# Kernel optimization log

Measured on AMD Instinct MI355X. Metric: run time of the kernel, lower is better.

The kernel has to match this reference:

```python
import jax, jax.numpy as jnp
import numpy as np

B, C, H, W = 8, 64, 64, 64
T, G, HID = 8, 8, 64


def setup_inputs() -> dict:
    key = jax.random.key(0)
    ks = jax.random.split(key, 8)
    s = 0.05
    return {
        "h": jax.random.normal(ks[0], (B, C, H, W), jnp.float32),
        "w_in": jax.random.normal(ks[1], (G * T, C), jnp.float32) * s,
        "b_in": jnp.zeros((G * T,), jnp.float32),
        "w_ih": jax.random.normal(ks[2], (4 * HID, 1), jnp.float32) * s,
        "w_hh": jax.random.normal(ks[3], (4 * HID, HID), jnp.float32) * s,
        "b_ih": jnp.zeros((4 * HID,), jnp.float32),
        "b_hh": jnp.zeros((4 * HID,), jnp.float32),
        "w_s": jax.random.normal(ks[4], (1, HID), jnp.float32) * s,
        "b_s": jnp.zeros((1,), jnp.float32),
        "w_out": jax.random.normal(ks[5], (C, G * T), jnp.float32) * s,
        "b_out": jnp.zeros((C,), jnp.float32),
    }


def reference(h, w_in, b_in, w_ih, w_hh, b_ih, b_hh, w_s, b_s, w_out, b_out):
    Bb, Cc, Hh, Ww = h.shape
    # 1x1 conv in-projection: (B,C,H,W) -> (B,G*T,H,W)
    y = jnp.einsum('bchw,oc->bohw', h, w_in) + b_in[None, :, None, None]
    y = y.reshape(Bb, G, T, Hh, Ww)
    # (B,G,H,W,T) -> (N,T) scalar sequences
    seq = jnp.transpose(y, (0, 1, 3, 4, 2)).reshape(-1, T)
    N = seq.shape[0]
    xs = seq.T  # (T, N) time-major for scan
    bias = b_ih + b_hh  # (4H,)
    w_x = w_ih[:, 0]    # (4H,) scalar-input weights

    def step(carry, x_t):
        hprev, cprev = carry
        # gates: i, f, g, o in torch LSTM ordering
        gates = x_t[:, None] * w_x[None, :] + hprev @ w_hh.T + bias  # (N,4H)
        i, f, g, o = jnp.split(gates, 4, axis=1)
        i = jax.nn.sigmoid(i)
        f = jax.nn.sigmoid(f)
        o = jax.nn.sigmoid(o)
        g = jnp.tanh(g)
        c = f * cprev + i * g
        hn = o * jnp.tanh(c)
        s_t = hn @ w_s[0] + b_s[0]  # fused to_scalar: (N,)
        return (hn, c), s_t

    init = (jnp.zeros((N, HID), h.dtype), jnp.zeros((N, HID), h.dtype))
    _, s = jax.lax.scan(step, init, xs)  # s: (T, N)

    out = s.T.reshape(Bb, G, Hh, Ww, T)
    out = jnp.transpose(out, (0, 1, 4, 2, 3)).reshape(Bb, G * T, Hh, Ww)
    # 1x1 conv out-projection back to C channels
    out = jnp.einsum('bchw,oc->bohw', out, w_out) + b_out[None, :, None, None]
    return out
```

## Files before the change

kernel.cpp:

```cpp
#include <hip/hip_runtime.h>
#include <hip/hip_bf16.h>

#define HW    4096
#define BB    8
#define TT    8

constexpr int OFF_WFRAG = 0;
constexpr int OFF_WXB   = 12800;

constexpr float SI = -1.44269504088896340736f;
constexpr float SG =  2.88539008177792681472f;

typedef _Float16 halfx8 __attribute__((ext_vector_type(8)));
typedef _Float16 halfx4 __attribute__((ext_vector_type(4)));
typedef float    floatx4 __attribute__((ext_vector_type(4)));
typedef float    floatx2 __attribute__((ext_vector_type(2)));

__device__ inline float fast_exp2(float x) {
#if __has_builtin(__builtin_amdgcn_exp2f)
    return __builtin_amdgcn_exp2f(x);
#else
    return __builtin_exp2f(x);
#endif
}
__device__ inline float fast_rcp(float x) {
#if __has_builtin(__builtin_amdgcn_rcpf)
    return __builtin_amdgcn_rcpf(x);
#else
    return 1.0f / x;
#endif
}
__device__ inline floatx2 exp2x2(floatx2 x) {
    floatx2 r; r.x = fast_exp2(x.x); r.y = fast_exp2(x.y); return r;
}
__device__ inline floatx2 rcpx2(floatx2 x) {
    float R = fast_rcp(x.x * x.y);
    floatx2 r; r.x = R * x.y; r.y = R * x.x; return r;
}

union pack8 { _Float16 h[8]; uint4 u; };

__global__ __launch_bounds__(256) void prep_kernel(
    const float* __restrict__ w_ih,  const float* __restrict__ w_hh,
    const float* __restrict__ b_ih,  const float* __restrict__ b_hh,
    const float* __restrict__ w_s,   const float* __restrict__ w_out,
    float* __restrict__ ws_f) {
    int tid = threadIdx.x;
    int bid = blockIdx.x;
    if (bid < 9) {
        int e = bid * 256 + tid;
        uint4* wf = (uint4*)(ws_f + OFF_WFRAG);
        if (e < 2048) {
            int l  = e & 63;
            int fi = e >> 6;
            int nb = fi >> 1, kc = fi & 1;
            int hb = nb & 3, gi = nb >> 2;
            int gate = gi * 64 + 4 * (l & 15) + hb;
            int hid  = kc * 32 + (l >> 4) * 8;
            float sc = (gi == 2) ? SG : SI;
            const float* src = w_hh + gate * 64 + hid;
            pack8 p;
            #pragma unroll
            for (int j = 0; j < 8; ++j) p.h[j] = (_Float16)(src[j] * sc);
            wf[e] = p.u;
        } else if (e < 2176) {
            int t2 = e - 2048;
            int l = t2 & 63, kc = t2 >> 6;
            pack8 p;
            #pragma unroll
            for (int j = 0; j < 8; ++j) p.h[j] = (_Float16)0.0f;
            if ((l & 15) == 0) {
                #pragma unroll
                for (int j = 0; j < 8; ++j)
                    p.h[j] = (_Float16)w_s[kc * 32 + (l >> 4) * 8 + j];
            }
            wf[e] = p.u;
        }
    } else {
        int s_ = tid & 15, hb = (tid >> 4) & 3, gi = tid >> 6;
        int gate = gi * 64 + 4 * s_ + hb;
        float sc = (gi == 2) ? SG : SI;
        floatx2 v; v.x = w_ih[gate] * sc; v.y = (b_ih[gate] + b_hh[gate]) * sc;
        ((floatx2*)(ws_f + OFF_WXB))[tid] = v;
    }
}

__global__ __launch_bounds__(512) void lstm_kernel(
    const float* __restrict__ hin,
    const float* __restrict__ ws_f,
    float* __restrict__ out,
    const float* __restrict__ w_in,
    const float* __restrict__ b_in,
    const float* __restrict__ b_s_p,
    const float* __restrict__ b_out,
    const float* __restrict__ w_out) {
    __shared__ uint4 wfrag_lds[2176];
    __shared__ floatx2 wxb_lds[256];
    __shared__ __align__(16) float x_lds[1024];
    __shared__ __align__(16) _Float16 h_lds[9216];
    __shared__ __align__(16) float stile[1024];
    __shared__ __align__(16) float wt_lds[4096];

    int tid = threadIdx.x;
    int ptile = blockIdx.x & 255;
    int b     = blockIdx.x >> 8;
    int p0 = ptile * 16;

    int lane = tid & 63;
    int wv   = tid >> 6;
    int g    = wv;
    int s    = lane & 15;
    int q    = lane >> 4;

    const uint4* wfg = (const uint4*)(ws_f + OFF_WFRAG);
    #pragma unroll
    for (int i = 0; i < 5; ++i) {
        int e = tid + 512 * i;
        if (e < 2176) wfrag_lds[e] = wfg[e];
    }
    if (tid < 256) wxb_lds[tid] = ((const floatx2*)(ws_f + OFF_WXB))[tid];
    #pragma unroll
    for (int i = 0; i < 2; ++i)
        ((floatx4*)wt_lds)[tid + 512 * i] = ((const floatx4*)w_in)[tid + 512 * i];
    if (tid < 256) {
        int cc = tid >> 2, f4 = tid & 3;
        ((floatx4*)stile)[tid] = *(const floatx4*)&hin[(b * 64 + cc) * HW + p0 + f4 * 4];
    }
    __syncthreads();

    {
        floatx2 xacc; xacc.x = b_in[g * 8 + q]; xacc.y = b_in[g * 8 + q + 4];
        #pragma unroll 8
        for (int cc = 0; cc < 64; ++cc) {
            float hv = stile[cc * 16 + s];
            floatx2 w;
            w.x = wt_lds[(g * 8 + q) * 64 + cc];
            w.y = wt_lds[(g * 8 + q + 4) * 64 + cc];
            floatx2 h2; h2.x = hv; h2.y = hv;
            xacc = xacc + w * h2;
        }
        x_lds[g * 128 + q * 16 + s]       = xacc.x;
        x_lds[g * 128 + (q + 4) * 16 + s] = xacc.y;
    }
    #pragma unroll
    for (int i = 0; i < 9; ++i)
        ((unsigned*)h_lds)[tid + 512 * i] = 0u;
    __syncthreads();

    #pragma unroll
    for (int i = 0; i < 2; ++i)
        ((floatx4*)wt_lds)[tid + 512 * i] = ((const floatx4*)w_out)[tid + 512 * i];

    _Float16* hrow = h_lds + wv * 16 * 72;
    float bs = b_s_p[0];

    float c_st[4][4];
    #pragma unroll
    for (int hb = 0; hb < 4; ++hb)
        #pragma unroll
        for (int r = 0; r < 4; ++r) c_st[hb][r] = 0.0f;

    for (int t = 0; t < TT; ++t) {
        asm volatile("" ::: "memory");

        halfx8 a0 = *(const halfx8*)(hrow + s * 72 + q * 8);
        halfx8 a1 = *(const halfx8*)(hrow + s * 72 + q * 8 + 32);

        if (t > 0) {
            halfx8 sb0 = *(const halfx8*)&wfrag_lds[32 * 64 + lane];
            halfx8 sb1 = *(const halfx8*)&wfrag_lds[33 * 64 + lane];
            floatx4 sa = {0.f, 0.f, 0.f, 0.f};
            sa = __builtin_amdgcn_mfma_f32_16x16x32_f16(a0, sb0, sa, 0, 0, 0);
            sa = __builtin_amdgcn_mfma_f32_16x16x32_f16(a1, sb1, sa, 0, 0, 0);
            if (s == 0) {
                floatx4 o4 = {sa[0] + bs, sa[1] + bs, sa[2] + bs, sa[3] + bs};
                *(floatx4*)&stile[(g * 8 + (t - 1)) * 16 + q * 4] = o4;
            }
        }

        floatx4 xv = *(const floatx4*)&x_lds[g * 128 + t * 16 + q * 4];
        floatx2 xlo; xlo.x = xv[0]; xlo.y = xv[1];
        floatx2 xhi; xhi.x = xv[2]; xhi.y = xv[3];

        halfx4 hpack[4];

        #pragma unroll
        for (int hb = 0; hb < 4; ++hb) {
            floatx4 acc[4];
            #pragma unroll
            for (int gi = 0; gi < 4; ++gi) {
                int nb = hb + 4 * gi;
                floatx2 wb = wxb_lds[s + 16 * nb];
                floatx2 lo = xlo * wb.x + wb.y;
                floatx2 hi = xhi * wb.x + wb.y;
                floatx4 a = {lo.x, lo.y, hi.x, hi.y};
                halfx8 b0 = *(const halfx8*)&wfrag_lds[(nb * 2 + 0) * 64 + lane];
                halfx8 b1 = *(const halfx8*)&wfrag_lds[(nb * 2 + 1) * 64 + lane];
                a = __builtin_amdgcn_mfma_f32_16x16x32_f16(a0, b0, a, 0, 0, 0);
                a = __builtin_amdgcn_mfma_f32_16x16x32_f16(a1, b1, a, 0, 0, 0);
                acc[gi] = a;
            }
            #pragma unroll
            for (int p = 0; p < 2; ++p) {
                int r0 = 2 * p;
                floatx2 Ei; Ei.x = fast_exp2(acc[0][r0]); Ei.y = fast_exp2(acc[0][r0 + 1]);
                floatx2 Ef; Ef.x = fast_exp2(acc[1][r0]); Ef.y = fast_exp2(acc[1][r0 + 1]);
                floatx2 Eg; Eg.x = fast_exp2(acc[2][r0]); Eg.y = fast_exp2(acc[2][r0 + 1]);
                floatx2 Eo; Eo.x = fast_exp2(acc[3][r0]); Eo.y = fast_exp2(acc[3][r0 + 1]);
                floatx2 Bf  = Ef + 1.0f;
                floatx2 Pig = (Ei + 1.0f) * (Eg + 1.0f);
                floatx2 cp; cp.x = c_st[hb][r0]; cp.y = c_st[hb][r0 + 1];
                floatx2 num = cp * Pig + (Eg * SG - SG) * Bf;
                floatx2 cs  = num * rcpx2(Bf * Pig);
                c_st[hb][r0] = cs.x; c_st[hb][r0 + 1] = cs.y;
                floatx2 Ec  = exp2x2(cs);
                floatx2 hn  = (Ec - 1.0f) * rcpx2((Eo + 1.0f) * (Ec + 1.0f));
                hpack[r0 + 0][hb] = (_Float16)hn.x;
                hpack[r0 + 1][hb] = (_Float16)hn.y;
            }
        }
        {
            _Float16* wp = hrow + (q * 4) * 72 + 4 * s;
            *(halfx4*)(wp +   0) = hpack[0];
            *(halfx4*)(wp +  72) = hpack[1];
            *(halfx4*)(wp + 144) = hpack[2];
            *(halfx4*)(wp + 216) = hpack[3];
        }
    }
    {
        asm volatile("" ::: "memory");
        halfx8 a0 = *(const halfx8*)(hrow + s * 72 + q * 8);
        halfx8 a1 = *(const halfx8*)(hrow + s * 72 + q * 8 + 32);
        halfx8 sb0 = *(const halfx8*)&wfrag_lds[32 * 64 + lane];
        halfx8 sb1 = *(const halfx8*)&wfrag_lds[33 * 64 + lane];
        floatx4 sa = {0.f, 0.f, 0.f, 0.f};
        sa = __builtin_amdgcn_mfma_f32_16x16x32_f16(a0, sb0, sa, 0, 0, 0);
        sa = __builtin_amdgcn_mfma_f32_16x16x32_f16(a1, sb1, sa, 0, 0, 0);
        if (s == 0) {
            floatx4 o4 = {sa[0] + bs, sa[1] + bs, sa[2] + bs, sa[3] + bs};
            *(floatx4*)&stile[(g * 8 + 7) * 16 + q * 4] = o4;
        }
    }
    __syncthreads();

    {
        int px = tid & 15;
        int oo = tid >> 4;
        floatx2 acc; acc.x = b_out[oo]; acc.y = b_out[oo + 32];
        #pragma unroll
        for (int c4 = 0; c4 < 16; ++c4) {
            floatx4 w0 = *(const floatx4*)&wt_lds[oo * 64 + c4 * 4];
            floatx4 w1 = *(const floatx4*)&wt_lds[(oo + 32) * 64 + c4 * 4];
            #pragma unroll
            for (int j = 0; j < 4; ++j) {
                float sv = stile[(c4 * 4 + j) * 16 + px];
                acc.x += w0[j] * sv;
                acc.y += w1[j] * sv;
            }
        }
        out[(b * 64 + oo) * HW + p0 + px]      = acc.x;
        out[(b * 64 + oo + 32) * HW + p0 + px] = acc.y;
    }
}

extern "C" void kernel_launch(void* const* d_in, const int* in_sizes, int n_in,
                              void* d_out, int out_size, void* d_ws, size_t ws_size,
                              hipStream_t stream) {
    const float* h     = (const float*)d_in[0];
    const float* w_in  = (const float*)d_in[1];
    const float* b_in  = (const float*)d_in[2];
    const float* w_ih  = (const float*)d_in[3];
    const float* w_hh  = (const float*)d_in[4];
    const float* b_ih  = (const float*)d_in[5];
    const float* b_hh  = (const float*)d_in[6];
    const float* w_s   = (const float*)d_in[7];
    const float* b_s   = (const float*)d_in[8];
    const float* w_out = (const float*)d_in[9];
    const float* b_out = (const float*)d_in[10];
    float* out = (float*)d_out;
    float* ws  = (float*)d_ws;

    prep_kernel<<<10, 256, 0, stream>>>(w_ih, w_hh, b_ih, b_hh, w_s, w_out, ws);
    lstm_kernel<<<2048, 512, 0, stream>>>(h, ws, out, w_in, b_in, b_s, b_out, w_out);
}
```

Baseline: 226.3 us.

## Process two pixel tiles per 1024-thread block with XOR-swizzled h buffer

Each block now handles two 16-pixel tiles using 1024 threads, so the LSTM weight fragments staged in LDS are shared across twice the work and the block count halves. The padded h layout is replaced by an XOR-swizzled 64-wide layout to avoid bank conflicts while using less padding. The w_in and w_out matrices are no longer staged in LDS and are read from global/cache directly, and the input and scalar-output tiles share a single buffer. The trade-off is larger blocks with more register and LDS pressure per block, plus uncached global weight reads in the projection loops.

```diff
diff --git a/kernel.cpp b/kernel.cpp
--- a/kernel.cpp
+++ b/kernel.cpp
@@ -85,7 +85,7 @@
     }
 }
 
-__global__ __launch_bounds__(512) void lstm_kernel(
+__global__ __launch_bounds__(1024) void lstm_kernel(
     const float* __restrict__ hin,
     const float* __restrict__ ws_f,
     float* __restrict__ out,
@@ -96,63 +96,62 @@
     const float* __restrict__ w_out) {
     __shared__ uint4 wfrag_lds[2176];
     __shared__ floatx2 wxb_lds[256];
-    __shared__ __align__(16) float x_lds[1024];
-    __shared__ __align__(16) _Float16 h_lds[9216];
-    __shared__ __align__(16) float stile[1024];
-    __shared__ __align__(16) float wt_lds[4096];
+    __shared__ __align__(16) float xs_buf[2048];
+    __shared__ __align__(16) _Float16 h_lds[16384];
 
     int tid = threadIdx.x;
-    int ptile = blockIdx.x & 255;
-    int b     = blockIdx.x >> 8;
-    int p0 = ptile * 16;
-
     int lane = tid & 63;
     int wv   = tid >> 6;
-    int g    = wv;
+    int tl   = wv >> 3;
+    int g    = wv & 7;
     int s    = lane & 15;
     int q    = lane >> 4;
 
+    int gt = blockIdx.x * 2 + tl;
+    int b  = gt >> 8;
+    int p0 = (gt & 255) * 16;
+
     const uint4* wfg = (const uint4*)(ws_f + OFF_WFRAG);
     #pragma unroll
-    for (int i = 0; i < 5; ++i) {
-        int e = tid + 512 * i;
+    for (int i = 0; i < 3; ++i) {
+        int e = tid + 1024 * i;
         if (e < 2176) wfrag_lds[e] = wfg[e];
     }
     if (tid < 256) wxb_lds[tid] = ((const floatx2*)(ws_f + OFF_WXB))[tid];
-    #pragma unroll
-    for (int i = 0; i < 2; ++i)
-        ((floatx4*)wt_lds)[tid + 512 * i] = ((const floatx4*)w_in)[tid + 512 * i];
-    if (tid < 256) {
-        int cc = tid >> 2, f4 = tid & 3;
-        ((floatx4*)stile)[tid] = *(const floatx4*)&hin[(b * 64 + cc) * HW + p0 + f4 * 4];
-    }
-    __syncthreads();
-
+    if (tid < 512) {
+        int tls = tid >> 8, cc = (tid >> 2) & 63, f4 = tid & 3;
+        int gts = blockIdx.x * 2 + tls;
+        int bs_ = gts >> 8, p0s = (gts & 255) * 16;
+        ((floatx4*)h_lds)[tid] =
+            *(const floatx4*)&hin[(bs_ * 64 + cc) * HW + p0s + f4 * 4];
+    }
+    __syncthreads();
+
+    float* xs = xs_buf + tl * 1024 + g * 128;
     {
+        const float* hin_st = (const float*)h_lds + tl * 1024;
+        const float* wrow0 = w_in + (g * 8 + q) * 64;
+        const float* wrow1 = w_in + (g * 8 + q + 4) * 64;
         floatx2 xacc; xacc.x = b_in[g * 8 + q]; xacc.y = b_in[g * 8 + q + 4];
         #pragma unroll 8
         for (int cc = 0; cc < 64; ++cc) {
-            float hv = stile[cc * 16 + s];
-            floatx2 w;
-            w.x = wt_lds[(g * 8 + q) * 64 + cc];
-            w.y = wt_lds[(g * 8 + q + 4) * 64 + cc];
-            floatx2 h2; h2.x = hv; h2.y = hv;
-            xacc = xacc + w * h2;
-        }
-        x_lds[g * 128 + q * 16 + s]       = xacc.x;
-        x_lds[g * 128 + (q + 4) * 16 + s] = xacc.y;
-    }
+            float hv = hin_st[cc * 16 + s];
+            xacc.x += wrow0[cc] * hv;
+            xacc.y += wrow1[cc] * hv;
+        }
+        xs[q * 16 + s]       = xacc.x;
+        xs[(q + 4) * 16 + s] = xacc.y;
+    }
+    __syncthreads();
     #pragma unroll
-    for (int i = 0; i < 9; ++i)
-        ((unsigned*)h_lds)[tid + 512 * i] = 0u;
-    __syncthreads();
-
-    #pragma unroll
-    for (int i = 0; i < 2; ++i)
-        ((floatx4*)wt_lds)[tid + 512 * i] = ((const floatx4*)w_out)[tid + 512 * i];
-
-    _Float16* hrow = h_lds + wv * 16 * 72;
+    for (int i = 0; i < 8; ++i)
+        ((unsigned*)h_lds)[tid + 1024 * i] = 0u;
+    __syncthreads();
+
+    _Float16* hrow = h_lds + wv * 1024;
     float bs = b_s_p[0];
+    int sh8 = (s >> 1);
+    int so4 = 4 * (s & 1);
 
     float c_st[4][4];
     #pragma unroll
@@ -163,8 +162,8 @@
     for (int t = 0; t < TT; ++t) {
         asm volatile("" ::: "memory");
 
-        halfx8 a0 = *(const halfx8*)(hrow + s * 72 + q * 8);
-        halfx8 a1 = *(const halfx8*)(hrow + s * 72 + q * 8 + 32);
+        halfx8 a0 = *(const halfx8*)(hrow + s * 64 + 8 * (q ^ (s & 7)));
+        halfx8 a1 = *(const halfx8*)(hrow + s * 64 + 8 * ((q + 4) ^ (s & 7)));
 
         if (t > 0) {
             halfx8 sb0 = *(const halfx8*)&wfrag_lds[32 * 64 + lane];
@@ -174,11 +173,11 @@
             sa = __builtin_amdgcn_mfma_f32_16x16x32_f16(a1, sb1, sa, 0, 0, 0);
             if (s == 0) {
                 floatx4 o4 = {sa[0] + bs, sa[1] + bs, sa[2] + bs, sa[3] + bs};
-                *(floatx4*)&stile[(g * 8 + (t - 1)) * 16 + q * 4] = o4;
-            }
-        }
-
-        floatx4 xv = *(const floatx4*)&x_lds[g * 128 + t * 16 + q * 4];
+                *(floatx4*)&xs[(t - 1) * 16 + q * 4] = o4;
+            }
+        }
+
+        floatx4 xv = *(const floatx4*)&xs[t * 16 + q * 4];
         floatx2 xlo; xlo.x = xv[0]; xlo.y = xv[1];
         floatx2 xhi; xhi.x = xv[2]; xhi.y = xv[3];
 
@@ -220,17 +219,18 @@
             }
         }
         {
-            _Float16* wp = hrow + (q * 4) * 72 + 4 * s;
-            *(halfx4*)(wp +   0) = hpack[0];
-            *(halfx4*)(wp +  72) = hpack[1];
-            *(halfx4*)(wp + 144) = hpack[2];
-            *(halfx4*)(wp + 216) = hpack[3];
+            int rowb = q * 4;
+            #pragma unroll
+            for (int r = 0; r < 4; ++r) {
+                int row = rowb + r;
+                *(halfx4*)(hrow + row * 64 + 8 * (sh8 ^ (row & 7)) + so4) = hpack[r];
+            }
         }
     }
     {
         asm volatile("" ::: "memory");
-        halfx8 a0 = *(const halfx8*)(hrow + s * 72 + q * 8);
-        halfx8 a1 = *(const halfx8*)(hrow + s * 72 + q * 8 + 32);
+        halfx8 a0 = *(const halfx8*)(hrow + s * 64 + 8 * (q ^ (s & 7)));
+        halfx8 a1 = *(const halfx8*)(hrow + s * 64 + 8 * ((q + 4) ^ (s & 7)));
         halfx8 sb0 = *(const halfx8*)&wfrag_lds[32 * 64 + lane];
         halfx8 sb1 = *(const halfx8*)&wfrag_lds[33 * 64 + lane];
         floatx4 sa = {0.f, 0.f, 0.f, 0.f};
@@ -238,28 +238,32 @@
         sa = __builtin_amdgcn_mfma_f32_16x16x32_f16(a1, sb1, sa, 0, 0, 0);
         if (s == 0) {
             floatx4 o4 = {sa[0] + bs, sa[1] + bs, sa[2] + bs, sa[3] + bs};
-            *(floatx4*)&stile[(g * 8 + 7) * 16 + q * 4] = o4;
+            *(floatx4*)&xs[7 * 16 + q * 4] = o4;
         }
     }
     __syncthreads();
 
     {
-        int px = tid & 15;
-        int oo = tid >> 4;
+        int tle = tid >> 9;
+        int px  = tid & 15;
+        int oo  = (tid >> 4) & 31;
+        int gte = blockIdx.x * 2 + tle;
+        int be  = gte >> 8, p0e = (gte & 255) * 16;
+        const float* st = xs_buf + tle * 1024;
         floatx2 acc; acc.x = b_out[oo]; acc.y = b_out[oo + 32];
         #pragma unroll
         for (int c4 = 0; c4 < 16; ++c4) {
-            floatx4 w0 = *(const floatx4*)&wt_lds[oo * 64 + c4 * 4];
-            floatx4 w1 = *(const floatx4*)&wt_lds[(oo + 32) * 64 + c4 * 4];
+            floatx4 w0 = *(const floatx4*)&w_out[oo * 64 + c4 * 4];
+            floatx4 w1 = *(const floatx4*)&w_out[(oo + 32) * 64 + c4 * 4];
             #pragma unroll
             for (int j = 0; j < 4; ++j) {
-                float sv = stile[(c4 * 4 + j) * 16 + px];
+                float sv = st[(c4 * 4 + j) * 16 + px];
                 acc.x += w0[j] * sv;
                 acc.y += w1[j] * sv;
             }
         }
-        out[(b * 64 + oo) * HW + p0 + px]      = acc.x;
-        out[(b * 64 + oo + 32) * HW + p0 + px] = acc.y;
+        out[(be * 64 + oo) * HW + p0e + px]      = acc.x;
+        out[(be * 64 + oo + 32) * HW + p0e + px] = acc.y;
     }
 }
 
@@ -281,5 +285,5 @@
     float* ws  = (float*)d_ws;
 
     prep_kernel<<<10, 256, 0, stream>>>(w_ih, w_hh, b_ih, b_hh, w_s, w_out, ws);
-    lstm_kernel<<<2048, 512, 0, stream>>>(h, ws, out, w_in, b_in, b_s, b_out, w_out);
-}
+    lstm_kernel<<<1024, 1024, 0, stream>>>(h, ws, out, w_in, b_in, b_s, b_out, w_out);
+}
```

Result: slower. 246.5 us (+8.9%).
